# Kernel optimization log

Measured on AMD Instinct MI355X. Metric: run time of the kernel, lower is better.

Reference implementation:

```python
import jax, jax.numpy as jnp
import numpy as np

B = 65536      # total rows = env_batch(8192) * n_slave(8)
DIN = 256      # input_shape
H = 64         # slave_hidden_dim
A = 32         # attention_dim
NACT = 14      # n_actions
NS = 8         # n_slave


def setup_inputs() -> dict:
    key = jax.random.key(0)
    ks = jax.random.split(key, 12)
    s = 0.05
    return {
        "obs": jax.random.normal(ks[0], (B, DIN), jnp.float32),
        "hidden_state": jax.random.normal(ks[1], (B, H), jnp.float32),
        "enc_W": jax.random.normal(ks[2], (DIN, H), jnp.float32) * s,
        "enc_b": jnp.zeros((H,), jnp.float32),
        "gru_Wih": jax.random.normal(ks[3], (3 * H, H), jnp.float32) * s,
        "gru_Whh": jax.random.normal(ks[4], (3 * H, H), jnp.float32) * s,
        "gru_bih": jnp.zeros((3 * H,), jnp.float32),
        "gru_bhh": jnp.zeros((3 * H,), jnp.float32),
        "qW": jax.random.normal(ks[5], (H, A), jnp.float32) * s,
        "kW": jax.random.normal(ks[6], (H, A), jnp.float32) * s,
        "vW": jax.random.normal(ks[7], (H, A), jnp.float32) * s,
        "vb": jnp.zeros((A,), jnp.float32),
        "decW": jax.random.normal(ks[8], (H + A, NACT), jnp.float32) * s,
        "decb": jnp.zeros((NACT,), jnp.float32),
        "n_slave": NS,
    }


def reference(obs, hidden_state, enc_W, enc_b, gru_Wih, gru_Whh, gru_bih, gru_bhh,
              qW, kW, vW, vb, decW, decb, n_slave):
    # encoding + ReLU
    x = jax.nn.relu(obs @ enc_W + enc_b)                      # [B, H]
    # torch GRUCell: r,z,n gate order in weight rows
    gx = x @ gru_Wih.T + gru_bih                              # [B, 3H]
    gh = hidden_state @ gru_Whh.T + gru_bhh                   # [B, 3H]
    xr, xz, xn = jnp.split(gx, 3, axis=-1)
    hr, hz, hn = jnp.split(gh, 3, axis=-1)
    r = jax.nn.sigmoid(xr + hr)
    z = jax.nn.sigmoid(xz + hz)
    n = jnp.tanh(xn + r * hn)
    h_out = (1.0 - z) * n + z * hidden_state                  # [B, H]

    Ad = qW.shape[-1]
    q = (h_out @ qW).reshape(-1, n_slave, Ad)                 # [b, n, A]
    k = (h_out @ kW).reshape(-1, n_slave, Ad)
    v = jax.nn.relu(h_out @ vW + vb).reshape(-1, n_slave, Ad)

    # exclude-self attention == diagonal-masked softmax attention
    scores = jnp.einsum('bia,bja->bij', q, k) / jnp.sqrt(jnp.float32(Ad))
    eye = jnp.eye(n_slave, dtype=bool)
    scores = jnp.where(eye, jnp.float32(-1e9), scores)
    attn = jax.nn.softmax(scores, axis=-1)                    # [b, n, n]
    xatt = jnp.einsum('bij,bja->bia', attn, v).reshape(-1, Ad)  # [B, A]

    out = jnp.concatenate([h_out, xatt], axis=-1) @ decW + decb  # [B, n_actions]
    return (out, h_out)
```

## Files before the change

kernel.cpp:

```cpp
#include <hip/hip_runtime.h>


#define NACT 14
#define BTOT 65536

typedef unsigned int  u32;
typedef unsigned short u16;
using short8 = __attribute__((ext_vector_type(8))) short;
using f32x4  = __attribute__((ext_vector_type(4))) float;

#define ENC0 0
#define WIH0 16384
#define WHH0 28672
#define QKV0 40960
#define DEC0 47104
#define WTOT 48640

#define WIHL 0
#define WHHL 12288
#define QKVL 24576
#define DECL 30720
#define DATA0 32256
#define BIASL 69120
#define LDSU16 69632

__device__ __align__(16) u16   g_wbuf[WTOT];
__device__ __align__(16) float g_bias[256];

__device__ __forceinline__ u32 f2bf_rne(float f){
  u32 x = __float_as_uint(f);
  return (x + 0x7fffu + ((x >> 16) & 1u)) >> 16;
}
__device__ __forceinline__ u32 pk2(float a, float b){
  u32 d;
  asm("v_cvt_pk_bf16_f32 %0, %1, %2" : "=v"(d) : "v"(a), "v"(b));
  return d;
}
__device__ __forceinline__ float blo(u32 u){ return __uint_as_float(u << 16); }
__device__ __forceinline__ float bhi(u32 u){ return __uint_as_float(u & 0xffff0000u); }
__device__ __forceinline__ float sigm(float x){ return 1.0f / (1.0f + __expf(-x)); }
__device__ __forceinline__ float tanhp(float x){ return 1.0f - 2.0f / (__expf(2.0f * x) + 1.0f); }
__device__ __forceinline__ short8 as_s8(uint4 v){ union { uint4 u; short8 s; } x; x.u = v; return x.s; }

#define MFMA16(a,b,c) __builtin_amdgcn_mfma_f32_16x16x32_bf16((a),(b),(c),0,0,0)

__global__ void prep(const float* __restrict__ encW, const float* __restrict__ Wih,
                     const float* __restrict__ Whh,  const float* __restrict__ qW,
                     const float* __restrict__ kW,   const float* __restrict__ vW,
                     const float* __restrict__ decW, const float* __restrict__ bih,
                     const float* __restrict__ bhh)
{
  int j = blockIdx.x * 256 + threadIdx.x;
  if (blockIdx.x == 0) {
    int n = threadIdx.x & 63, g = threadIdx.x >> 6;
    float v;
    if      (g == 0) v = bih[n]       + bhh[n];
    else if (g == 1) v = bih[64 + n]  + bhh[64 + n];
    else if (g == 2) v = bih[128 + n];
    else             v = bhh[128 + n];
    g_bias[threadIdx.x] = v;
  }
  if (j >= WTOT) return;
  int pos  = j & 511;
  int lane = pos >> 3, jj = pos & 7;
  int quad = lane >> 4, l16 = lane & 15;
  float val = 0.f;
  if (j < WIH0) {
    int f = j >> 9, ks = f >> 2, t = f & 3;
    int k = ks * 32 + quad * 8 + jj, n = 16 * t + l16;
    val = encW[k * 64 + n];
  } else if (j < WHH0) {
    int f = (j - WIH0) >> 9;
    int u = f / 6, g = (f >> 1) % 3, ks = f & 1;
    int wrow = 64 * g + 16 * u + l16, k = ks * 32 + quad * 8 + jj;
    val = Wih[wrow * 64 + k];
  } else if (j < QKV0) {
    int f = (j - WHH0) >> 9;
    int u = f / 6, g = (f >> 1) % 3, ks = f & 1;
    int wrow = 64 * g + 16 * u + l16, k = ks * 32 + quad * 8 + jj;
    val = Whh[wrow * 64 + k];
  } else if (j < DEC0) {
    int f = (j - QKV0) >> 9, t = f >> 1, ks = f & 1;
    int n = 16 * t + l16, mtx = n >> 5, nn = n & 31;
    int k = ks * 32 + quad * 8 + jj;
    val = (mtx == 0) ? qW[k * 32 + nn] * 0.17677669529663687f
        : (mtx == 1) ? kW[k * 32 + nn] : vW[k * 32 + nn];
  } else {
    int f = (j - DEC0) >> 9;
    int k = f * 32 + quad * 8 + jj, n = l16;
    if (n < 14) val = decW[k * 14 + n];
  }
  g_wbuf[j] = (u16)f2bf_rne(val);
}

struct Chunk {
  float4 ob[16];
  float4 hv[4];
};

__device__ __forceinline__ void issue_loads(int gr, const float* __restrict__ obs,
                                            const float* __restrict__ hid,
                                            int lane, int quad, int l16, Chunk& c)
{
  const float* ap = obs + (size_t)(gr + l16) * 256 + quad * 8;
  #pragma unroll
  for (int ks = 0; ks < 8; ks++) {
    c.ob[2 * ks]     = *(const float4*)(ap + ks * 32);
    c.ob[2 * ks + 1] = *(const float4*)(ap + ks * 32 + 4);
  }
  #pragma unroll
  for (int i = 0; i < 4; i++) {
    int cc = lane + 64 * i;
    c.hv[i] = ((const float4*)hid)[(size_t)(gr + (cc >> 4)) * 16 + (cc & 15)];
  }
}

template<bool LAST>
__device__ __forceinline__ void tile_body(
    int gr, int grN,
    u16* __restrict__ Xb, const u16* __restrict__ wl, const float* __restrict__ biasL,
    const float* __restrict__ obs, const float* __restrict__ hid,
    const float* __restrict__ encb, const float* __restrict__ vb,
    const float* __restrict__ decb, float* __restrict__ out,
    Chunk& cur, Chunk& nxt,
    int lane, int quad, int l16)
{
  u16*   Hb = Xb + 1152;
  float* Sf = (float*)(Xb + 2304);

  #pragma unroll
  for (int i = 0; i < 4; i++) {
    int c = lane + 64 * i;
    int lr = c >> 4, c4 = c & 15;
    *(uint2*)&Hb[lr * 72 + c4 * 4] =
        make_uint2(pk2(cur.hv[i].x, cur.hv[i].y), pk2(cur.hv[i].z, cur.hv[i].w));
  }

  f32x4 ce[4];
  #pragma unroll
  for (int t = 0; t < 4; t++) {
    float bv = encb[16 * t + l16];
    ce[t] = (f32x4){bv, bv, bv, bv};
  }
  #pragma unroll
  for (int ks = 0; ks < 8; ks++) {
    float4 a0 = cur.ob[2 * ks], a1 = cur.ob[2 * ks + 1];
    short8 a = as_s8(make_uint4(pk2(a0.x, a0.y), pk2(a0.z, a0.w), pk2(a1.x, a1.y), pk2(a1.z, a1.w)));
    #pragma unroll
    for (int t = 0; t < 4; t++) {
      short8 b = as_s8(*(const uint4*)&g_wbuf[ENC0 + (ks * 4 + t) * 512 + lane * 8]);
      ce[t] = MFMA16(a, b, ce[t]);
    }
  }
  if (!LAST) issue_loads(grN, obs, hid, lane, quad, l16, nxt);
  #pragma unroll
  for (int t = 0; t < 4; t++)
    #pragma unroll
    for (int r = 0; r < 4; r++) {
      float xv = fmaxf(ce[t][r], 0.f);
      Xb[(quad * 4 + r) * 72 + 16 * t + l16] = (u16)pk2(xv, xv);
    }

  short8 ax[2], ah[2];
  #pragma unroll
  for (int ks = 0; ks < 2; ks++) {
    ax[ks] = *(const short8*)&Xb[l16 * 72 + ks * 32 + quad * 8];
    ah[ks] = *(const short8*)&Hb[l16 * 72 + ks * 32 + quad * 8];
  }
  #pragma unroll
  for (int u = 0; u < 4; u++) {
    f32x4 g6[6];
    #pragma unroll
    for (int t = 0; t < 6; t++) g6[t] = (f32x4){0.f, 0.f, 0.f, 0.f};
    #pragma unroll
    for (int g = 0; g < 3; g++) {
      #pragma unroll
      for (int ks = 0; ks < 2; ks++) {
        int f = (u * 3 + g) * 2 + ks;
        short8 bi = *(const short8*)&wl[WIHL + f * 512 + lane * 8];
        short8 bh = *(const short8*)&wl[WHHL + f * 512 + lane * 8];
        g6[g]     = MFMA16(ax[ks], bi, g6[g]);
        g6[3 + g] = MFMA16(ah[ks], bh, g6[3 + g]);
      }
    }
    int nc = 16 * u + l16;
    float brz = biasL[nc], bzz = biasL[64 + nc], bni = biasL[128 + nc], bnh = biasL[192 + nc];
    float hp[4];
    #pragma unroll
    for (int r = 0; r < 4; r++)
      hp[r] = blo(Hb[(quad * 4 + r) * 72 + nc]);
    #pragma unroll
    for (int r = 0; r < 4; r++) {
      float rg = sigm(g6[0][r] + g6[3][r] + brz);
      float zg = sigm(g6[1][r] + g6[4][r] + bzz);
      float nn = tanhp(g6[2][r] + bni + rg * (g6[5][r] + bnh));
      float ho = (1.f - zg) * nn + zg * hp[r];
      Hb[(quad * 4 + r) * 72 + nc] = (u16)pk2(ho, ho);
    }
  }

  short8 hx[2];
  #pragma unroll
  for (int ks = 0; ks < 2; ks++)
    hx[ks] = *(const short8*)&Hb[l16 * 72 + ks * 32 + quad * 8];
  f32x4 cq[6];
  #pragma unroll
  for (int t = 0; t < 6; t++) {
    float bv = (t >= 4) ? vb[16 * (t - 4) + l16] : 0.f;
    cq[t] = (f32x4){bv, bv, bv, bv};
  }
  #pragma unroll
  for (int ks = 0; ks < 2; ks++)
    #pragma unroll
    for (int t = 0; t < 6; t++) {
      short8 b = *(const short8*)&wl[QKVL + (t * 2 + ks) * 512 + lane * 8];
      cq[t] = MFMA16(hx[ks], b, cq[t]);
    }
  #pragma unroll
  for (int t = 0; t < 4; t++)
    #pragma unroll
    for (int r = 0; r < 4; r++)
      Sf[(quad * 4 + r) * 68 + 16 * t + l16] = cq[t][r];
  #pragma unroll
  for (int t = 4; t < 6; t++)
    #pragma unroll
    for (int r = 0; r < 4; r++)
      Xb[(quad * 4 + r) * 72 + 32 + 16 * (t - 4) + l16] =
          (u16)pk2(fmaxf(cq[t][r], 0.f), 0.f);

  {
    const int r_l = lane >> 2, s4 = lane & 3;
    const int gb = r_l & ~7, ri = r_l & 7;
    const float* fq = &Sf[r_l * 68];
    float sc[2];
    #pragma unroll
    for (int jj = 0; jj < 2; jj++) {
      int j = 2 * s4 + jj;
      const float* fk = &Sf[(gb + j) * 68 + 32];
      float d = 0.f;
      #pragma unroll
      for (int a4 = 0; a4 < 32; a4 += 4) {
        float4 q4 = *(const float4*)&fq[a4];
        float4 k4 = *(const float4*)&fk[a4];
        d += q4.x * k4.x + q4.y * k4.y + q4.z * k4.z + q4.w * k4.w;
      }
      sc[jj] = (j == ri) ? -1e30f : d;
    }
    float m = fmaxf(sc[0], sc[1]);
    m = fmaxf(m, __shfl_xor(m, 1));
    m = fmaxf(m, __shfl_xor(m, 2));
    float p[2], sum = 0.f;
    #pragma unroll
    for (int jj = 0; jj < 2; jj++) {
      int j = 2 * s4 + jj;
      p[jj] = (j == ri) ? 0.f : __expf(sc[jj] - m);
      sum += p[jj];
    }
    sum += __shfl_xor(sum, 1);
    sum += __shfl_xor(sum, 2);
    float inv = 1.f / sum;
    #pragma unroll
    for (int jj = 0; jj < 2; jj++)
      Sf[r_l * 68 + 2 * s4 + jj] = p[jj] * inv;
    float xa[8];
    #pragma unroll
    for (int u = 0; u < 8; u++) xa[u] = 0.f;
    #pragma unroll
    for (int j = 0; j < 8; j++) {
      float aj = Sf[r_l * 68 + j];
      const u16* vp = &Xb[(gb + j) * 72 + 32 + 8 * s4];
      uint4 v0 = *(const uint4*)vp;
      xa[0] += aj * blo(v0.x); xa[1] += aj * bhi(v0.x);
      xa[2] += aj * blo(v0.y); xa[3] += aj * bhi(v0.y);
      xa[4] += aj * blo(v0.z); xa[5] += aj * bhi(v0.z);
      xa[6] += aj * blo(v0.w); xa[7] += aj * bhi(v0.w);
    }
    u16* xp = &Xb[r_l * 72 + 8 * s4];
    *(uint4*)xp = make_uint4(pk2(xa[0], xa[1]), pk2(xa[2], xa[3]),
                             pk2(xa[4], xa[5]), pk2(xa[6], xa[7]));
  }

  {
    float db = (l16 < NACT) ? decb[l16] : 0.f;
    f32x4 co = (f32x4){db, db, db, db};
    #pragma unroll
    for (int ks = 0; ks < 2; ks++) {
      short8 b = *(const short8*)&wl[DECL + ks * 512 + lane * 8];
      short8 a = *(const short8*)&Hb[l16 * 72 + ks * 32 + quad * 8];
      co = MFMA16(a, b, co);
    }
    short8 b2 = *(const short8*)&wl[DECL + 2 * 512 + lane * 8];
    short8 a2 = *(const short8*)&Xb[l16 * 72 + quad * 8];
    co = MFMA16(a2, b2, co);
    if (l16 < NACT)
      #pragma unroll
      for (int r = 0; r < 4; r++)
        out[(size_t)(gr + quad * 4 + r) * NACT + l16] = co[r];
  }

  {
    float* outH = out + (size_t)BTOT * NACT;
    #pragma unroll
    for (int i = 0; i < 2; i++) {
      int c = lane + 64 * i, lr = c >> 3, j = c & 7;
      uint4 u = *(const uint4*)&Hb[lr * 72 + 8 * j];
      *(float4*)(outH + (size_t)(gr + lr) * 64 + 8 * j) =
          make_float4(blo(u.x), bhi(u.x), blo(u.y), bhi(u.y));
      *(float4*)(outH + (size_t)(gr + lr) * 64 + 8 * j + 4) =
          make_float4(blo(u.z), bhi(u.z), blo(u.w), bhi(u.w));
    }
  }
}

__global__ __launch_bounds__(512, 2)
void commslave_main(const float* __restrict__ obs,  const float* __restrict__ hid,
                    const float* __restrict__ encb, const float* __restrict__ vb,
                    const float* __restrict__ decb, float* __restrict__ out)
{
  __shared__ __align__(16) u16 lds[LDSU16];

  const int tid  = threadIdx.x;
  const int w    = tid >> 6;
  const int lane = tid & 63;
  const int quad = lane >> 4;
  const int l16  = lane & 15;

  const int gr0 = blockIdx.x * 256 + w * 16;
  const int gr1 = gr0 + 128;

  Chunk c0, c1;
  issue_loads(gr0, obs, hid, lane, quad, l16, c0);

  {
    uint4* dw = (uint4*)lds;
    const uint4* sw = (const uint4*)(g_wbuf + WIH0);
    #pragma unroll
    for (int i = 0; i < 8; i++) {
      int idx = tid + 512 * i;
      if (idx < 4032) dw[idx] = sw[idx];
    }
    if (tid < 64) ((uint4*)(lds + BIASL))[tid] = ((const uint4*)g_bias)[tid];
  }
  __syncthreads();

  u16* Xb = lds + DATA0 + w * 4608;
  const float* biasL = (const float*)(lds + BIASL);

  tile_body<false>(gr0, gr1, Xb, lds, biasL, obs, hid, encb, vb, decb, out,
                   c0, c1, lane, quad, l16);
  tile_body<true >(gr1, 0,   Xb, lds, biasL, obs, hid, encb, vb, decb, out,
                   c1, c0, lane, quad, l16);
}

extern "C" void kernel_launch(void* const* d_in, const int* in_sizes, int n_in,
                              void* d_out, int out_size, void* d_ws, size_t ws_size,
                              hipStream_t stream) {
  (void)in_sizes; (void)n_in; (void)d_ws; (void)ws_size; (void)out_size;
  const float* obs  = (const float*)d_in[0];
  const float* hid  = (const float*)d_in[1];
  const float* encW = (const float*)d_in[2];
  const float* encb = (const float*)d_in[3];
  const float* Wih  = (const float*)d_in[4];
  const float* Whh  = (const float*)d_in[5];
  const float* bih  = (const float*)d_in[6];
  const float* bhh  = (const float*)d_in[7];
  const float* qW   = (const float*)d_in[8];
  const float* kW   = (const float*)d_in[9];
  const float* vW   = (const float*)d_in[10];
  const float* vb   = (const float*)d_in[11];
  const float* decW = (const float*)d_in[12];
  const float* decb = (const float*)d_in[13];
  float* out = (float*)d_out;

  prep<<<(WTOT + 255) / 256, 256, 0, stream>>>(encW, Wih, Whh, qW, kW, vW, decW, bih, bhh);
  commslave_main<<<256, 512, 0, stream>>>(obs, hid, encb, vb, decb, out);
}
```

Measured before the change: 144.8 us.

## Interleave second tile's encoder with first tile's GRU/attention and raise MFMA priority

Splits the per-tile body into stages and reorders them so the second tile's encoder MFMAs (into a new per-wave X2 LDS buffer) run between the first tile's GRU/QKV and attention/decoder stages. The aim is more independent work per wave, so MFMA and LDS/VALU latency can overlap. It also wraps MFMA blocks in s_setprio to favour matrix issue across waves. The cost is a larger per-wave LDS footprint (5760 vs 4608 u16), which could reduce occupancy, plus register pressure from holding both chunks' data live.

```diff
diff --git a/kernel.cpp b/kernel.cpp
--- a/kernel.cpp
+++ b/kernel.cpp
@@ -21,8 +21,12 @@
 #define QKVL 24576
 #define DECL 30720
 #define DATA0 32256
-#define BIASL 69120
-#define LDSU16 69632
+#define HOFF 1152
+#define SFO  2304
+#define X2OFF 4608
+#define WAVEU16 5760
+#define BIASL 78336
+#define LDSU16 78848
 
 __device__ __align__(16) u16   g_wbuf[WTOT];
 __device__ __align__(16) float g_bias[256];
@@ -115,27 +119,22 @@
   }
 }
 
-template<bool LAST>
-__device__ __forceinline__ void tile_body(
-    int gr, int grN,
-    u16* __restrict__ Xb, const u16* __restrict__ wl, const float* __restrict__ biasL,
-    const float* __restrict__ obs, const float* __restrict__ hid,
-    const float* __restrict__ encb, const float* __restrict__ vb,
-    const float* __restrict__ decb, float* __restrict__ out,
-    Chunk& cur, Chunk& nxt,
-    int lane, int quad, int l16)
-{
-  u16*   Hb = Xb + 1152;
-  float* Sf = (float*)(Xb + 2304);
-
+__device__ __forceinline__ void hid_stage(u16* __restrict__ Hb, const Chunk& c, int lane)
+{
   #pragma unroll
   for (int i = 0; i < 4; i++) {
-    int c = lane + 64 * i;
-    int lr = c >> 4, c4 = c & 15;
+    int cc = lane + 64 * i;
+    int lr = cc >> 4, c4 = cc & 15;
     *(uint2*)&Hb[lr * 72 + c4 * 4] =
-        make_uint2(pk2(cur.hv[i].x, cur.hv[i].y), pk2(cur.hv[i].z, cur.hv[i].w));
-  }
-
+        make_uint2(pk2(c.hv[i].x, c.hv[i].y), pk2(c.hv[i].z, c.hv[i].w));
+  }
+}
+
+__device__ __forceinline__ void enc_front(u16* __restrict__ Xdst,
+                                          const float* __restrict__ encb,
+                                          const Chunk& cur,
+                                          int lane, int quad, int l16)
+{
   f32x4 ce[4];
   #pragma unroll
   for (int t = 0; t < 4; t++) {
@@ -152,19 +151,28 @@
       ce[t] = MFMA16(a, b, ce[t]);
     }
   }
-  if (!LAST) issue_loads(grN, obs, hid, lane, quad, l16, nxt);
   #pragma unroll
   for (int t = 0; t < 4; t++)
     #pragma unroll
     for (int r = 0; r < 4; r++) {
       float xv = fmaxf(ce[t][r], 0.f);
-      Xb[(quad * 4 + r) * 72 + 16 * t + l16] = (u16)pk2(xv, xv);
-    }
-
+      Xdst[(quad * 4 + r) * 72 + 16 * t + l16] = (u16)pk2(xv, xv);
+    }
+}
+
+__device__ __forceinline__ void gru_qkv(const u16* __restrict__ Xsrc,
+                                        u16* __restrict__ Xv,
+                                        u16* __restrict__ Hb,
+                                        float* __restrict__ Sf,
+                                        const u16* __restrict__ wl,
+                                        const float* __restrict__ biasL,
+                                        const float* __restrict__ vb,
+                                        int lane, int quad, int l16)
+{
   short8 ax[2], ah[2];
   #pragma unroll
   for (int ks = 0; ks < 2; ks++) {
-    ax[ks] = *(const short8*)&Xb[l16 * 72 + ks * 32 + quad * 8];
+    ax[ks] = *(const short8*)&Xsrc[l16 * 72 + ks * 32 + quad * 8];
     ah[ks] = *(const short8*)&Hb[l16 * 72 + ks * 32 + quad * 8];
   }
   #pragma unroll
@@ -172,6 +180,7 @@
     f32x4 g6[6];
     #pragma unroll
     for (int t = 0; t < 6; t++) g6[t] = (f32x4){0.f, 0.f, 0.f, 0.f};
+    __builtin_amdgcn_s_setprio(1);
     #pragma unroll
     for (int g = 0; g < 3; g++) {
       #pragma unroll
@@ -183,6 +192,7 @@
         g6[3 + g] = MFMA16(ah[ks], bh, g6[3 + g]);
       }
     }
+    __builtin_amdgcn_s_setprio(0);
     int nc = 16 * u + l16;
     float brz = biasL[nc], bzz = biasL[64 + nc], bni = biasL[128 + nc], bnh = biasL[192 + nc];
     float hp[4];
@@ -209,6 +219,7 @@
     float bv = (t >= 4) ? vb[16 * (t - 4) + l16] : 0.f;
     cq[t] = (f32x4){bv, bv, bv, bv};
   }
+  __builtin_amdgcn_s_setprio(1);
   #pragma unroll
   for (int ks = 0; ks < 2; ks++)
     #pragma unroll
@@ -216,6 +227,7 @@
       short8 b = *(const short8*)&wl[QKVL + (t * 2 + ks) * 512 + lane * 8];
       cq[t] = MFMA16(hx[ks], b, cq[t]);
     }
+  __builtin_amdgcn_s_setprio(0);
   #pragma unroll
   for (int t = 0; t < 4; t++)
     #pragma unroll
@@ -225,9 +237,19 @@
   for (int t = 4; t < 6; t++)
     #pragma unroll
     for (int r = 0; r < 4; r++)
-      Xb[(quad * 4 + r) * 72 + 32 + 16 * (t - 4) + l16] =
+      Xv[(quad * 4 + r) * 72 + 32 + 16 * (t - 4) + l16] =
           (u16)pk2(fmaxf(cq[t][r], 0.f), 0.f);
-
+}
+
+__device__ __forceinline__ void attn_dec(int gr,
+                                         u16* __restrict__ Xb,
+                                         const u16* __restrict__ Hb,
+                                         float* __restrict__ Sf,
+                                         const u16* __restrict__ wl,
+                                         const float* __restrict__ decb,
+                                         float* __restrict__ out,
+                                         int lane, int quad, int l16)
+{
   {
     const int r_l = lane >> 2, s4 = lane & 3;
     const int gb = r_l & ~7, ri = r_l & 7;
@@ -283,6 +305,7 @@
   {
     float db = (l16 < NACT) ? decb[l16] : 0.f;
     f32x4 co = (f32x4){db, db, db, db};
+    __builtin_amdgcn_s_setprio(1);
     #pragma unroll
     for (int ks = 0; ks < 2; ks++) {
       short8 b = *(const short8*)&wl[DECL + ks * 512 + lane * 8];
@@ -292,6 +315,7 @@
     short8 b2 = *(const short8*)&wl[DECL + 2 * 512 + lane * 8];
     short8 a2 = *(const short8*)&Xb[l16 * 72 + quad * 8];
     co = MFMA16(a2, b2, co);
+    __builtin_amdgcn_s_setprio(0);
     if (l16 < NACT)
       #pragma unroll
       for (int r = 0; r < 4; r++)
@@ -302,7 +326,7 @@
     float* outH = out + (size_t)BTOT * NACT;
     #pragma unroll
     for (int i = 0; i < 2; i++) {
-      int c = lane + 64 * i, lr = c >> 3, j = c & 7;
+      int cc = lane + 64 * i, lr = cc >> 3, j = cc & 7;
       uint4 u = *(const uint4*)&Hb[lr * 72 + 8 * j];
       *(float4*)(outH + (size_t)(gr + lr) * 64 + 8 * j) =
           make_float4(blo(u.x), bhi(u.x), blo(u.y), bhi(u.y));
@@ -343,13 +367,21 @@
   }
   __syncthreads();
 
-  u16* Xb = lds + DATA0 + w * 4608;
+  u16*   Xb    = lds + DATA0 + w * WAVEU16;
+  u16*   Hb    = Xb + HOFF;
+  u16*   X2    = Xb + X2OFF;
+  float* Sf    = (float*)(Xb + SFO);
   const float* biasL = (const float*)(lds + BIASL);
 
-  tile_body<false>(gr0, gr1, Xb, lds, biasL, obs, hid, encb, vb, decb, out,
-                   c0, c1, lane, quad, l16);
-  tile_body<true >(gr1, 0,   Xb, lds, biasL, obs, hid, encb, vb, decb, out,
-                   c1, c0, lane, quad, l16);
+  hid_stage(Hb, c0, lane);
+  enc_front(Xb, encb, c0, lane, quad, l16);
+  issue_loads(gr1, obs, hid, lane, quad, l16, c1);
+  gru_qkv(Xb, Xb, Hb, Sf, lds, biasL, vb, lane, quad, l16);
+  enc_front(X2, encb, c1, lane, quad, l16);
+  attn_dec(gr0, Xb, Hb, Sf, lds, decb, out, lane, quad, l16);
+  hid_stage(Hb, c1, lane);
+  gru_qkv(X2, Xb, Hb, Sf, lds, biasL, vb, lane, quad, l16);
+  attn_dec(gr1, Xb, Hb, Sf, lds, decb, out, lane, quad, l16);
 }
 
 extern "C" void kernel_launch(void* const* d_in, const int* in_sizes, int n_in,
```

New measurement: 146.8 us. About the same (+1.4%).
